# Kernel optimization log

Hardware: AMD Instinct MI355X
Metric: run time of the kernel (lower is better)

The kernel has to match this reference:

```python
import jax, jax.numpy as jnp
import numpy as np

N_NODES = 50000
N_EDGES = 800000
HEADS = 4
HID = 48
NEG_SLOPE = 0.2


def setup_inputs() -> dict:
    key = jax.random.key(0)
    ks = list(jax.random.split(key, 32))
    inp = {}
    inp['x'] = jax.random.normal(ks[0], (N_NODES, 3), dtype=jnp.float32)
    inp['edge_index'] = jax.random.randint(ks[1], (2, N_EDGES), 0, N_NODES, dtype=jnp.int64)
    dims = [3, HID, HID]
    ki = 2
    for li, din in enumerate(dims):
        s = 1.0 / np.sqrt(din)
        inp[f'Wl{li}'] = jax.random.normal(ks[ki], (din, HEADS * HID), dtype=jnp.float32) * s; ki += 1
        inp[f'bl{li}'] = jnp.zeros((HEADS * HID,), dtype=jnp.float32)
        inp[f'Wr{li}'] = jax.random.normal(ks[ki], (din, HEADS * HID), dtype=jnp.float32) * s; ki += 1
        inp[f'br{li}'] = jnp.zeros((HEADS * HID,), dtype=jnp.float32)
        inp[f'att{li}'] = jax.random.normal(ks[ki], (HEADS, HID), dtype=jnp.float32) * (1.0 / np.sqrt(HID)); ki += 1
        inp[f'bias{li}'] = jnp.zeros((HID,), dtype=jnp.float32)
    inp['head_w'] = jax.random.normal(ks[ki], (HID, 1), dtype=jnp.float32) * (1.0 / np.sqrt(HID))
    inp['head_b'] = jnp.full((1,), 0.1, dtype=jnp.float32)
    return inp


def _gatv2_layer(x, src, dst, Wl, bl, Wr, br, att, bias):
    # GATv2Conv, concat=False, eval mode (dropout off), self-loops already in (src,dst)
    N = x.shape[0]
    xl = (x @ Wl + bl).reshape(N, HEADS, HID)  # source transform
    xr = (x @ Wr + br).reshape(N, HEADS, HID)  # target transform
    e = jax.nn.leaky_relu(xl[src] + xr[dst], NEG_SLOPE)  # [E,H,C]
    score = jnp.einsum('ehc,hc->eh', e, att)             # [E,H]
    # segment softmax over edges grouped by destination node
    m = jax.ops.segment_max(score, dst, num_segments=N)
    p = jnp.exp(score - m[dst])
    denom = jax.ops.segment_sum(p, dst, num_segments=N)
    alpha = p / (denom[dst] + 1e-16)                     # [E,H]
    out = jax.ops.segment_sum(alpha[..., None] * xl[src], dst, num_segments=N)  # [N,H,C]
    return out.mean(axis=1) + bias  # concat=False -> mean over heads


def reference(x, edge_index, Wl0, bl0, Wr0, br0, att0, bias0,
              Wl1, bl1, Wr1, br1, att1, bias1,
              Wl2, bl2, Wr2, br2, att2, bias2, head_w, head_b):
    N = x.shape[0]
    loops = jnp.arange(N, dtype=edge_index.dtype)
    src = jnp.concatenate([edge_index[0], loops])  # PyG add_self_loops=True
    dst = jnp.concatenate([edge_index[1], loops])
    params = [(Wl0, bl0, Wr0, br0, att0, bias0),
              (Wl1, bl1, Wr1, br1, att1, bias1),
              (Wl2, bl2, Wr2, br2, att2, bias2)]
    for (Wl, bl, Wr, br, att, bias) in params:
        x = _gatv2_layer(x, src, dst, Wl, bl, Wr, br, att, bias)
        x = jax.nn.elu(x)
    out = (x @ head_w + head_b)[:, 0]
    return jax.nn.relu(out)
```

## Files before the change

### kernel.cpp

```cpp
#include <hip/hip_runtime.h>
#include <hip/hip_bf16.h>
#include <math.h>

#define HEADS 4
#define HID 48
#define FDIM 192
#define NEG_SLOPE 0.2f

typedef float f4 __attribute__((ext_vector_type(4)));

template<int CTRL>
__device__ __forceinline__ float dpp_add(float v) {
    int t = __builtin_amdgcn_update_dpp(0, __float_as_int(v), CTRL, 0xF, 0xF, true);
    return v + __int_as_float(t);
}
template<int CTRL>
__device__ __forceinline__ float dpp_max(float v) {
    int t = __builtin_amdgcn_update_dpp(0, __float_as_int(v), CTRL, 0xF, 0xF, true);
    return fmaxf(v, __int_as_float(t));
}
__device__ __forceinline__ float red_cq(float v) {
    v = dpp_add<0xB1>(v);
    v = dpp_add<0x4E>(v);
    return v;
}
__device__ __forceinline__ float red_es(float v) {
    v = dpp_add<0x124>(v);
    v = dpp_add<0x128>(v);
    return v;
}
__device__ __forceinline__ float rowmax16(float v) {
    v = dpp_max<0x124>(v);
    v = dpp_max<0x128>(v);
    return v;
}

__device__ __forceinline__ int detect64(const int* __restrict__ ei) {
    int l = (int)(threadIdx.x & 63);
    int v = ei[2 * l + 1];
    return (__ballot(v != 0) == 0ULL) ? 1 : 0;
}

__global__ void hist_kernel(const int* __restrict__ ei,
                            int* __restrict__ deg, int E, int E2) {
    int is64 = detect64(ei);
    for (int e = blockIdx.x * blockDim.x + threadIdx.x; e < E2;
         e += gridDim.x * blockDim.x) {
        int d;
        if (e < E) d = is64 ? ei[2 * (E + e)] : ei[E + e];
        else       d = e - E;
        atomicAdd(&deg[d], 1);
    }
}

__global__ void scan_local_kernel(const int* __restrict__ deg, int* __restrict__ incl,
                                  int* __restrict__ bsum, int N) {
    __shared__ int sm[256];
    int i = blockIdx.x * 256 + threadIdx.x;
    int v = (i < N) ? deg[i] : 0;
    sm[threadIdx.x] = v;
    __syncthreads();
    #pragma unroll
    for (int off = 1; off < 256; off <<= 1) {
        int t = ((int)threadIdx.x >= off) ? sm[threadIdx.x - off] : 0;
        __syncthreads();
        sm[threadIdx.x] += t;
        __syncthreads();
    }
    if (i < N) incl[i] = sm[threadIdx.x];
    if (threadIdx.x == 255) bsum[blockIdx.x] = sm[255];
}

__global__ void scan_bsum_kernel(int* __restrict__ bsum, int nb) {
    __shared__ int sm[256];
    __shared__ int running;
    if (threadIdx.x == 0) running = 0;
    __syncthreads();
    for (int base = 0; base < nb; base += 256) {
        int i = base + (int)threadIdx.x;
        int v = (i < nb) ? bsum[i] : 0;
        sm[threadIdx.x] = v;
        __syncthreads();
        #pragma unroll
        for (int off = 1; off < 256; off <<= 1) {
            int t = ((int)threadIdx.x >= off) ? sm[threadIdx.x - off] : 0;
            __syncthreads();
            sm[threadIdx.x] += t;
            __syncthreads();
        }
        if (i < nb) bsum[i] = running + sm[threadIdx.x] - v;
        __syncthreads();
        if (threadIdx.x == 0) running += sm[255];
        __syncthreads();
    }
}

__global__ void scan_final_kernel(const int* __restrict__ incl, const int* __restrict__ bsum,
                                  int* __restrict__ rowptr, int* __restrict__ cursor, int N) {
    int i = blockIdx.x * 256 + threadIdx.x;
    if (i < N) { rowptr[i + 1] = incl[i] + bsum[blockIdx.x]; cursor[i] = 0; }
    if (i == 0) rowptr[0] = 0;
}

__global__ void scatter_kernel(const int* __restrict__ ei,
                               const int* __restrict__ rowptr, int* __restrict__ cursor,
                               int* __restrict__ srcs, int E, int E2) {
    int is64 = detect64(ei);
    for (int e = blockIdx.x * blockDim.x + threadIdx.x; e < E2;
         e += gridDim.x * blockDim.x) {
        int s, d;
        if (e < E) {
            if (is64) { s = ei[2 * e]; d = ei[2 * (E + e)]; }
            else      { s = ei[e];     d = ei[E + e]; }
        } else {
            s = d = e - E;
        }
        int pos = rowptr[d] + atomicAdd(&cursor[d], 1);
        srcs[pos] = s;
    }
}

template<int DIN>
__global__ __launch_bounds__(192) void gemm2t_kernel(
    const float* __restrict__ xin,
    const float* __restrict__ Wl, const float* __restrict__ bl,
    const float* __restrict__ Wr, const float* __restrict__ br,
    float* __restrict__ xl, float* __restrict__ xr, int N) {
    int t  = (int)threadIdx.x;
    int cg = t % 48;
    int ng = t / 48;
    int c0 = cg * 4;
    int n0 = blockIdx.x * 16 + ng * 4;
    if (n0 >= N) return;

    f4 bLv = *(const f4*)&bl[c0];
    f4 bRv = *(const f4*)&br[c0];
    f4 accL[4], accR[4];
    #pragma unroll
    for (int i = 0; i < 4; ++i) { accL[i] = bLv; accR[i] = bRv; }

    if (n0 + 3 < N) {
        if (DIN == 3) {
            float xv[4][3];
            #pragma unroll
            for (int i = 0; i < 4; ++i) {
                const float* xp = xin + (size_t)(n0 + i) * 3;
                xv[i][0] = xp[0]; xv[i][1] = xp[1]; xv[i][2] = xp[2];
            }
            #pragma unroll
            for (int k = 0; k < 3; ++k) {
                f4 wl4 = *(const f4*)&Wl[k * FDIM + c0];
                f4 wr4 = *(const f4*)&Wr[k * FDIM + c0];
                #pragma unroll
                for (int i = 0; i < 4; ++i) {
                    float xs = xv[i][k];
                    accL[i] += xs * wl4;
                    accR[i] += xs * wr4;
                }
            }
        } else {
            #pragma unroll
            for (int kk = 0; kk < DIN; kk += 8) {
                float xv[4][8];
                #pragma unroll
                for (int i = 0; i < 4; ++i) {
                    const float* xp = xin + (size_t)(n0 + i) * DIN + kk;
                    f4 xa = *(const f4*)xp;
                    f4 xb = *(const f4*)(xp + 4);
                    #pragma unroll
                    for (int q = 0; q < 4; ++q) { xv[i][q] = xa[q]; xv[i][4 + q] = xb[q]; }
                }
                #pragma unroll
                for (int k = 0; k < 8; ++k) {
                    f4 wl4 = *(const f4*)&Wl[(kk + k) * FDIM + c0];
                    f4 wr4 = *(const f4*)&Wr[(kk + k) * FDIM + c0];
                    #pragma unroll
                    for (int i = 0; i < 4; ++i) {
                        float xs = xv[i][k];
                        accL[i] += xs * wl4;
                        accR[i] += xs * wr4;
                    }
                }
            }
        }
        #pragma unroll
        for (int i = 0; i < 4; ++i) {
            *(f4*)&xl[(size_t)(n0 + i) * FDIM + c0] = accL[i];
            *(f4*)&xr[(size_t)(n0 + i) * FDIM + c0] = accR[i];
        }
    } else {
        for (int i = 0; i < 4; ++i) {
            int n = n0 + i;
            if (n >= N) break;
            f4 aL = bLv;
            f4 aR = bRv;
            for (int k = 0; k < DIN; ++k) {
                float xs = xin[(size_t)n * DIN + k];
                f4 wl4 = *(const f4*)&Wl[k * FDIM + c0];
                f4 wr4 = *(const f4*)&Wr[k * FDIM + c0];
                aL += xs * wl4;
                aR += xs * wr4;
            }
            *(f4*)&xl[(size_t)n * FDIM + c0] = aL;
            *(f4*)&xr[(size_t)n * FDIM + c0] = aR;
        }
    }
}

#define SCORE_MASKED (-1e38f)
#define M_INIT       (-3e38f)
#define DEFER_THR    8.0f

__global__ __launch_bounds__(256) void gat_layer_kernel(
    const float* __restrict__ xl, const float* __restrict__ xr,
    const float* __restrict__ att, const float* __restrict__ bias,
    const int* __restrict__ rowptr, const int* __restrict__ srcs,
    float* __restrict__ xout,
    float* __restrict__ out,
    const float* __restrict__ head_w, const float* __restrict__ head_b,
    int N, int final_flag) {
    int wave = (int)((blockIdx.x * blockDim.x + threadIdx.x) >> 6);
    wave = __builtin_amdgcn_readfirstlane(wave);
    if (wave >= N) return;
    int lane = (int)(threadIdx.x & 63);
    int n  = wave;
    int h  = lane >> 4;
    int es = (lane >> 2) & 3;
    int cq = lane & 3;
    int j0 = h * HID + cq * 12;

    const float* xrp = xr + (size_t)n * FDIM + j0;
    f4 r0 = *(const f4*)xrp;
    f4 r1 = *(const f4*)(xrp + 4);
    f4 r2 = *(const f4*)(xrp + 8);
    f4 a0 = *(const f4*)&att[j0];
    f4 a1 = *(const f4*)&att[j0 + 4];
    f4 a2 = *(const f4*)&att[j0 + 8];

    float m = M_INIT, dn = 0.f;
    f4 acc0 = {0.f, 0.f, 0.f, 0.f}, acc1 = acc0, acc2 = acc0;

    int e0 = rowptr[n], e1 = rowptr[n + 1];
    int elast = e1 - 1;

    for (int e = e0; e < e1; e += 8) {
        int iA = e + es;
        int iB = e + 4 + es;
        int kA = (iA < e1) ? iA : elast;
        int kB = (iB < e1) ? iB : elast;
        int sA = srcs[kA];
        int sB = srcs[kB];
        const float* pA = xl + (size_t)sA * FDIM + j0;
        const float* pB = xl + (size_t)sB * FDIM + j0;
        f4 A0 = *(const f4*)pA, A1 = *(const f4*)(pA + 4), A2 = *(const f4*)(pA + 8);
        f4 B0 = *(const f4*)pB, B1 = *(const f4*)(pB + 4), B2 = *(const f4*)(pB + 8);

        float scA = 0.f, scB = 0.f;
        #pragma unroll
        for (int q = 0; q < 4; ++q) {
            float t, u;
            t = A0[q] + r0[q]; u = fmaf(NEG_SLOPE, fminf(t, 0.f), fmaxf(t, 0.f)); scA = fmaf(u, a0[q], scA);
            t = A1[q] + r1[q]; u = fmaf(NEG_SLOPE, fminf(t, 0.f), fmaxf(t, 0.f)); scA = fmaf(u, a1[q], scA);
            t = A2[q] + r2[q]; u = fmaf(NEG_SLOPE, fminf(t, 0.f), fmaxf(t, 0.f)); scA = fmaf(u, a2[q], scA);
            t = B0[q] + r0[q]; u = fmaf(NEG_SLOPE, fminf(t, 0.f), fmaxf(t, 0.f)); scB = fmaf(u, a0[q], scB);
            t = B1[q] + r1[q]; u = fmaf(NEG_SLOPE, fminf(t, 0.f), fmaxf(t, 0.f)); scB = fmaf(u, a1[q], scB);
            t = B2[q] + r2[q]; u = fmaf(NEG_SLOPE, fminf(t, 0.f), fmaxf(t, 0.f)); scB = fmaf(u, a2[q], scB);
        }
        scA = red_cq(scA);
        scB = red_cq(scB);
        scA = (iA < e1) ? scA : SCORE_MASKED;
        scB = (iB < e1) ? scB : SCORE_MASKED;

        float bmax = rowmax16(fmaxf(scA, scB));
        if (__any(bmax > m + DEFER_THR)) {
            float nm = fmaxf(m, bmax);
            float sc_ = __expf(m - nm);
            dn *= sc_; acc0 *= sc_; acc1 *= sc_; acc2 *= sc_;
            m = nm;
        }
        float qA = __expf(scA - m);
        float qB = __expf(scB - m);
        dn += qA + qB;
        acc0 += qA * A0 + qB * B0;
        acc1 += qA * A1 + qB * B1;
        acc2 += qA * A2 + qB * B2;
    }

    dn = red_es(dn);
    #pragma unroll
    for (int q = 0; q < 4; ++q) {
        acc0[q] = red_es(acc0[q]);
        acc1[q] = red_es(acc1[q]);
        acc2[q] = red_es(acc2[q]);
    }

    float inv = 1.0f / (dn + 1e-16f);
    f4 o0 = acc0 * inv, o1 = acc1 * inv, o2 = acc2 * inv;

    #pragma unroll
    for (int q = 0; q < 4; ++q) {
        float v;
        v = o0[q]; v += __shfl_xor(v, 16); v += __shfl_xor(v, 32); o0[q] = v;
        v = o1[q]; v += __shfl_xor(v, 16); v += __shfl_xor(v, 32); o1[q] = v;
        v = o2[q]; v += __shfl_xor(v, 16); v += __shfl_xor(v, 32); o2[q] = v;
    }
    int c0 = cq * 12;
    f4 b0v = *(const f4*)&bias[c0];
    f4 b1v = *(const f4*)&bias[c0 + 4];
    f4 b2v = *(const f4*)&bias[c0 + 8];
    o0 = 0.25f * o0 + b0v;
    o1 = 0.25f * o1 + b1v;
    o2 = 0.25f * o2 + b2v;
    #pragma unroll
    for (int q = 0; q < 4; ++q) {
        o0[q] = (o0[q] > 0.f) ? o0[q] : (__expf(o0[q]) - 1.f);
        o1[q] = (o1[q] > 0.f) ? o1[q] : (__expf(o1[q]) - 1.f);
        o2[q] = (o2[q] > 0.f) ? o2[q] : (__expf(o2[q]) - 1.f);
    }

    if (!final_flag) {
        if (h == 0 && es == 0) {
            float* xo = xout + (size_t)n * HID + c0;
            *(f4*)xo = o0;
            *(f4*)(xo + 4) = o1;
            *(f4*)(xo + 8) = o2;
        }
    } else {
        f4 w0 = *(const f4*)&head_w[c0];
        f4 w1 = *(const f4*)&head_w[c0 + 4];
        f4 w2 = *(const f4*)&head_w[c0 + 8];
        float part = 0.f;
        #pragma unroll
        for (int q = 0; q < 4; ++q)
            part += o0[q] * w0[q] + o1[q] * w1[q] + o2[q] * w2[q];
        part = red_cq(part);
        if (lane == 0) {
            float v = part + head_b[0];
            out[n] = (v > 0.f) ? v : 0.f;
        }
    }
}

extern "C" void kernel_launch(void* const* d_in, const int* in_sizes, int n_in,
                              void* d_out, int out_size, void* d_ws, size_t ws_size,
                              hipStream_t stream) {
    const float* x0 = (const float*)d_in[0];
    const int*   ei = (const int*)d_in[1];

    const int N  = in_sizes[0] / 3;
    const int E  = in_sizes[1] / 2;
    const int E2 = E + N;

    const float* Wl[3];  const float* bl[3];
    const float* Wr[3];  const float* br[3];
    const float* att[3]; const float* bias[3];
    for (int li = 0; li < 3; ++li) {
        int b = 2 + 6 * li;
        Wl[li]   = (const float*)d_in[b + 0];
        bl[li]   = (const float*)d_in[b + 1];
        Wr[li]   = (const float*)d_in[b + 2];
        br[li]   = (const float*)d_in[b + 3];
        att[li]  = (const float*)d_in[b + 4];
        bias[li] = (const float*)d_in[b + 5];
    }
    const float* head_w = (const float*)d_in[20];
    const float* head_b = (const float*)d_in[21];
    float* out = (float*)d_out;

    size_t off = 0;
    auto alloc = [&](size_t bytes) -> void* {
        void* p = (char*)d_ws + off;
        off = (off + bytes + 255) & ~(size_t)255;
        return p;
    };
    const int nb = (N + 255) / 256;
    int*   deg    = (int*)alloc((size_t)N * sizeof(int));
    int*   incl   = (int*)alloc((size_t)N * sizeof(int));
    int*   bsum   = (int*)alloc((size_t)nb * sizeof(int));
    int*   rowptr = (int*)alloc((size_t)(N + 1) * sizeof(int));
    int*   srcs   = (int*)alloc((size_t)E2 * sizeof(int));
    float* xlb    = (float*)alloc((size_t)N * FDIM * sizeof(float));
    float* xrb    = (float*)alloc((size_t)N * FDIM * sizeof(float));
    float* xbuf   = (float*)alloc((size_t)N * HID * sizeof(float));
    (void)ws_size;

    (void)hipMemsetAsync(deg, 0, (size_t)N * sizeof(int), stream);
    hist_kernel<<<2048, 256, 0, stream>>>(ei, deg, E, E2);
    scan_local_kernel<<<nb, 256, 0, stream>>>(deg, incl, bsum, N);
    scan_bsum_kernel<<<1, 256, 0, stream>>>(bsum, nb);
    scan_final_kernel<<<nb, 256, 0, stream>>>(incl, bsum, rowptr, deg, N);
    scatter_kernel<<<2048, 256, 0, stream>>>(ei, rowptr, deg, srcs, E, E2);

    const int waves_per_block = 4;
    int gat_blocks = (N + waves_per_block - 1) / waves_per_block;
    int gemm_blocks = (N + 15) / 16;

    gemm2t_kernel<3><<<gemm_blocks, 192, 0, stream>>>(x0, Wl[0], bl[0], Wr[0], br[0], xlb, xrb, N);
    gat_layer_kernel<<<gat_blocks, 256, 0, stream>>>(xlb, xrb, att[0], bias[0],
        rowptr, srcs, xbuf, nullptr, nullptr, nullptr, N, 0);

    gemm2t_kernel<HID><<<gemm_blocks, 192, 0, stream>>>(xbuf, Wl[1], bl[1], Wr[1], br[1], xlb, xrb, N);
    gat_layer_kernel<<<gat_blocks, 256, 0, stream>>>(xlb, xrb, att[1], bias[1],
        rowptr, srcs, xbuf, nullptr, nullptr, nullptr, N, 0);

    gemm2t_kernel<HID><<<gemm_blocks, 192, 0, stream>>>(xbuf, Wl[2], bl[2], Wr[2], br[2], xlb, xrb, N);
    gat_layer_kernel<<<gat_blocks, 256, 0, stream>>>(xlb, xrb, att[2], bias[2],
        rowptr, srcs, nullptr, out, head_w, head_b, N, 1);

    (void)n_in; (void)out_size;
}
```

Baseline: 490.2 us.

## Split GAT aggregation per head with head-major layout and XCD-aware block mapping

The projected features are stored head-major ([H][N][48]) instead of node-major, and the aggregation is split so each block handles a single head. Block IDs are mapped so that each pair of XCDs works on one head, which keeps each XCD's gather working set (one head's slice of xl) small enough to fit in its L2. Per-head partial results are combined with atomicAdd into a zeroed buffer. Separate combine kernels then apply bias and ELU, plus the output head in the last layer. The cost is extra launches and memsets, float atomics with non-deterministic summation order, and one edge per lane-group per iteration instead of two.

Result: slower. 1.571 ms (+220.5%).

```diff
diff --git a/kernel.cpp b/kernel.cpp
--- a/kernel.cpp
+++ b/kernel.cpp
@@ -24,14 +24,14 @@
     v = dpp_add<0x4E>(v);
     return v;
 }
-__device__ __forceinline__ float red_es(float v) {
-    v = dpp_add<0x124>(v);
-    v = dpp_add<0x128>(v);
-    return v;
-}
 __device__ __forceinline__ float rowmax16(float v) {
     v = dpp_max<0x124>(v);
     v = dpp_max<0x128>(v);
+    return v;
+}
+__device__ __forceinline__ float rowadd16(float v) {
+    v = dpp_add<0x124>(v);
+    v = dpp_add<0x128>(v);
     return v;
 }
 
@@ -132,6 +132,8 @@
     int c0 = cg * 4;
     int n0 = blockIdx.x * 16 + ng * 4;
     if (n0 >= N) return;
+    int hh = c0 / 48;
+    int ch = c0 - hh * 48;
 
     f4 bLv = *(const f4*)&bl[c0];
     f4 bRv = *(const f4*)&br[c0];
@@ -185,8 +187,9 @@
         }
         #pragma unroll
         for (int i = 0; i < 4; ++i) {
-            *(f4*)&xl[(size_t)(n0 + i) * FDIM + c0] = accL[i];
-            *(f4*)&xr[(size_t)(n0 + i) * FDIM + c0] = accR[i];
+            size_t o = ((size_t)hh * N + (n0 + i)) * HID + ch;
+            *(f4*)&xl[o] = accL[i];
+            *(f4*)&xr[o] = accR[i];
         }
     } else {
         for (int i = 0; i < 4; ++i) {
@@ -201,8 +204,9 @@
                 aL += xs * wl4;
                 aR += xs * wr4;
             }
-            *(f4*)&xl[(size_t)n * FDIM + c0] = aL;
-            *(f4*)&xr[(size_t)n * FDIM + c0] = aR;
+            size_t o = ((size_t)hh * N + n) * HID + ch;
+            *(f4*)&xl[o] = aL;
+            *(f4*)&xr[o] = aR;
         }
     }
 }
@@ -211,133 +215,149 @@
 #define M_INIT       (-3e38f)
 #define DEFER_THR    8.0f
 
-__global__ __launch_bounds__(256) void gat_layer_kernel(
-    const float* __restrict__ xl, const float* __restrict__ xr,
-    const float* __restrict__ att, const float* __restrict__ bias,
+__global__ __launch_bounds__(256) void gat_head_kernel(
+    const float* __restrict__ xlh,
+    const float* __restrict__ xrh,
+    const float* __restrict__ att,
     const int* __restrict__ rowptr, const int* __restrict__ srcs,
-    float* __restrict__ xout,
-    float* __restrict__ out,
-    const float* __restrict__ head_w, const float* __restrict__ head_b,
-    int N, int final_flag) {
-    int wave = (int)((blockIdx.x * blockDim.x + threadIdx.x) >> 6);
-    wave = __builtin_amdgcn_readfirstlane(wave);
-    if (wave >= N) return;
+    float* __restrict__ psum,
+    int N) {
+    int bid = (int)blockIdx.x;
+    int xcd = bid & 7;
+    int h   = xcd >> 1;
+    int j   = (bid >> 3) * 2 + (xcd & 1);
+    int wv  = (int)(threadIdx.x >> 6);
     int lane = (int)(threadIdx.x & 63);
-    int n  = wave;
-    int h  = lane >> 4;
-    int es = (lane >> 2) & 3;
-    int cq = lane & 3;
-    int j0 = h * HID + cq * 12;
-
-    const float* xrp = xr + (size_t)n * FDIM + j0;
+    int half = lane >> 5;
+    int l5 = lane & 31;
+    int es = l5 >> 2;
+    int cq = l5 & 3;
+    int c0 = cq * 12;
+    int n = j * 8 + wv * 2 + half;
+    bool nvalid = (n < N);
+    int nc = nvalid ? n : 0;
+
+    const float* hb = xlh + (size_t)h * N * HID;
+    const float* xrp = xrh + (size_t)h * N * HID + (size_t)nc * HID + c0;
     f4 r0 = *(const f4*)xrp;
     f4 r1 = *(const f4*)(xrp + 4);
     f4 r2 = *(const f4*)(xrp + 8);
-    f4 a0 = *(const f4*)&att[j0];
-    f4 a1 = *(const f4*)&att[j0 + 4];
-    f4 a2 = *(const f4*)&att[j0 + 8];
+    f4 a0 = *(const f4*)&att[h * HID + c0];
+    f4 a1 = *(const f4*)&att[h * HID + c0 + 4];
+    f4 a2 = *(const f4*)&att[h * HID + c0 + 8];
+
+    int e0 = nvalid ? rowptr[n] : 0;
+    int e1 = nvalid ? rowptr[n + 1] : 0;
+    int elast = e1 - 1;
 
     float m = M_INIT, dn = 0.f;
     f4 acc0 = {0.f, 0.f, 0.f, 0.f}, acc1 = acc0, acc2 = acc0;
 
-    int e0 = rowptr[n], e1 = rowptr[n + 1];
-    int elast = e1 - 1;
-
     for (int e = e0; e < e1; e += 8) {
-        int iA = e + es;
-        int iB = e + 4 + es;
-        int kA = (iA < e1) ? iA : elast;
-        int kB = (iB < e1) ? iB : elast;
-        int sA = srcs[kA];
-        int sB = srcs[kB];
-        const float* pA = xl + (size_t)sA * FDIM + j0;
-        const float* pB = xl + (size_t)sB * FDIM + j0;
-        f4 A0 = *(const f4*)pA, A1 = *(const f4*)(pA + 4), A2 = *(const f4*)(pA + 8);
-        f4 B0 = *(const f4*)pB, B1 = *(const f4*)(pB + 4), B2 = *(const f4*)(pB + 8);
-
-        float scA = 0.f, scB = 0.f;
+        int idx = e + es;
+        int k = (idx < e1) ? idx : elast;
+        int s = srcs[k];
+        const float* p = hb + (size_t)s * HID + c0;
+        f4 A0 = *(const f4*)p;
+        f4 A1 = *(const f4*)(p + 4);
+        f4 A2 = *(const f4*)(p + 8);
+
+        float sc = 0.f;
         #pragma unroll
         for (int q = 0; q < 4; ++q) {
-            float t, u;
-            t = A0[q] + r0[q]; u = fmaf(NEG_SLOPE, fminf(t, 0.f), fmaxf(t, 0.f)); scA = fmaf(u, a0[q], scA);
-            t = A1[q] + r1[q]; u = fmaf(NEG_SLOPE, fminf(t, 0.f), fmaxf(t, 0.f)); scA = fmaf(u, a1[q], scA);
-            t = A2[q] + r2[q]; u = fmaf(NEG_SLOPE, fminf(t, 0.f), fmaxf(t, 0.f)); scA = fmaf(u, a2[q], scA);
-            t = B0[q] + r0[q]; u = fmaf(NEG_SLOPE, fminf(t, 0.f), fmaxf(t, 0.f)); scB = fmaf(u, a0[q], scB);
-            t = B1[q] + r1[q]; u = fmaf(NEG_SLOPE, fminf(t, 0.f), fmaxf(t, 0.f)); scB = fmaf(u, a1[q], scB);
-            t = B2[q] + r2[q]; u = fmaf(NEG_SLOPE, fminf(t, 0.f), fmaxf(t, 0.f)); scB = fmaf(u, a2[q], scB);
-        }
-        scA = red_cq(scA);
-        scB = red_cq(scB);
-        scA = (iA < e1) ? scA : SCORE_MASKED;
-        scB = (iB < e1) ? scB : SCORE_MASKED;
-
-        float bmax = rowmax16(fmaxf(scA, scB));
+            float t;
+            t = A0[q] + r0[q]; sc = fmaf(fmaxf(t, NEG_SLOPE * t), a0[q], sc);
+            t = A1[q] + r1[q]; sc = fmaf(fmaxf(t, NEG_SLOPE * t), a1[q], sc);
+            t = A2[q] + r2[q]; sc = fmaf(fmaxf(t, NEG_SLOPE * t), a2[q], sc);
+        }
+        sc = red_cq(sc);
+        sc = (idx < e1) ? sc : SCORE_MASKED;
+
+        float bmax = rowmax16(sc);
+        bmax = fmaxf(bmax, __shfl_xor(bmax, 16));
         if (__any(bmax > m + DEFER_THR)) {
             float nm = fmaxf(m, bmax);
-            float sc_ = __expf(m - nm);
-            dn *= sc_; acc0 *= sc_; acc1 *= sc_; acc2 *= sc_;
+            float s_ = __expf(m - nm);
+            dn *= s_; acc0 *= s_; acc1 *= s_; acc2 *= s_;
             m = nm;
         }
-        float qA = __expf(scA - m);
-        float qB = __expf(scB - m);
-        dn += qA + qB;
-        acc0 += qA * A0 + qB * B0;
-        acc1 += qA * A1 + qB * B1;
-        acc2 += qA * A2 + qB * B2;
-    }
-
-    dn = red_es(dn);
-    #pragma unroll
-    for (int q = 0; q < 4; ++q) {
-        acc0[q] = red_es(acc0[q]);
-        acc1[q] = red_es(acc1[q]);
-        acc2[q] = red_es(acc2[q]);
-    }
-
-    float inv = 1.0f / (dn + 1e-16f);
-    f4 o0 = acc0 * inv, o1 = acc1 * inv, o2 = acc2 * inv;
-
+        float q_ = __expf(sc - m);
+        dn += q_;
+        acc0 += q_ * A0;
+        acc1 += q_ * A1;
+        acc2 += q_ * A2;
+    }
+
+    dn = rowadd16(dn); dn += __shfl_xor(dn, 16);
     #pragma unroll
     for (int q = 0; q < 4; ++q) {
         float v;
-        v = o0[q]; v += __shfl_xor(v, 16); v += __shfl_xor(v, 32); o0[q] = v;
-        v = o1[q]; v += __shfl_xor(v, 16); v += __shfl_xor(v, 32); o1[q] = v;
-        v = o2[q]; v += __shfl_xor(v, 16); v += __shfl_xor(v, 32); o2[q] = v;
-    }
+        v = rowadd16(acc0[q]); v += __shfl_xor(v, 16); acc0[q] = v;
+        v = rowadd16(acc1[q]); v += __shfl_xor(v, 16); acc1[q] = v;
+        v = rowadd16(acc2[q]); v += __shfl_xor(v, 16); acc2[q] = v;
+    }
+
+    if (nvalid && es == 0) {
+        float w = 0.25f / (dn + 1e-16f);
+        float* po = psum + (size_t)n * HID + c0;
+        #pragma unroll
+        for (int q = 0; q < 4; ++q) {
+            atomicAdd(&po[q],     acc0[q] * w);
+            atomicAdd(&po[4 + q], acc1[q] * w);
+            atomicAdd(&po[8 + q], acc2[q] * w);
+        }
+    }
+}
+
+__global__ void combine_kernel(float* __restrict__ psum,
+                               const float* __restrict__ bias, int N) {
+    int t = blockIdx.x * 256 + threadIdx.x;
+    int n = t >> 2, cq = t & 3;
+    if (n >= N) return;
     int c0 = cq * 12;
-    f4 b0v = *(const f4*)&bias[c0];
-    f4 b1v = *(const f4*)&bias[c0 + 4];
-    f4 b2v = *(const f4*)&bias[c0 + 8];
-    o0 = 0.25f * o0 + b0v;
-    o1 = 0.25f * o1 + b1v;
-    o2 = 0.25f * o2 + b2v;
+    float* p = psum + (size_t)n * HID + c0;
+    f4 v0 = *(const f4*)p + *(const f4*)&bias[c0];
+    f4 v1 = *(const f4*)(p + 4) + *(const f4*)&bias[c0 + 4];
+    f4 v2 = *(const f4*)(p + 8) + *(const f4*)&bias[c0 + 8];
     #pragma unroll
     for (int q = 0; q < 4; ++q) {
-        o0[q] = (o0[q] > 0.f) ? o0[q] : (__expf(o0[q]) - 1.f);
-        o1[q] = (o1[q] > 0.f) ? o1[q] : (__expf(o1[q]) - 1.f);
-        o2[q] = (o2[q] > 0.f) ? o2[q] : (__expf(o2[q]) - 1.f);
-    }
-
-    if (!final_flag) {
-        if (h == 0 && es == 0) {
-            float* xo = xout + (size_t)n * HID + c0;
-            *(f4*)xo = o0;
-            *(f4*)(xo + 4) = o1;
-            *(f4*)(xo + 8) = o2;
-        }
-    } else {
-        f4 w0 = *(const f4*)&head_w[c0];
-        f4 w1 = *(const f4*)&head_w[c0 + 4];
-        f4 w2 = *(const f4*)&head_w[c0 + 8];
-        float part = 0.f;
-        #pragma unroll
-        for (int q = 0; q < 4; ++q)
-            part += o0[q] * w0[q] + o1[q] * w1[q] + o2[q] * w2[q];
-        part = red_cq(part);
-        if (lane == 0) {
-            float v = part + head_b[0];
-            out[n] = (v > 0.f) ? v : 0.f;
-        }
+        v0[q] = (v0[q] > 0.f) ? v0[q] : (__expf(v0[q]) - 1.f);
+        v1[q] = (v1[q] > 0.f) ? v1[q] : (__expf(v1[q]) - 1.f);
+        v2[q] = (v2[q] > 0.f) ? v2[q] : (__expf(v2[q]) - 1.f);
+    }
+    *(f4*)p = v0;
+    *(f4*)(p + 4) = v1;
+    *(f4*)(p + 8) = v2;
+}
+
+__global__ void combine_final_kernel(const float* __restrict__ psum,
+                                     const float* __restrict__ bias,
+                                     const float* __restrict__ head_w,
+                                     const float* __restrict__ head_b,
+                                     float* __restrict__ out, int N) {
+    int t = blockIdx.x * 256 + threadIdx.x;
+    int n = t >> 2, cq = t & 3;
+    if (n >= N) return;
+    int c0 = cq * 12;
+    const float* p = psum + (size_t)n * HID + c0;
+    f4 v0 = *(const f4*)p + *(const f4*)&bias[c0];
+    f4 v1 = *(const f4*)(p + 4) + *(const f4*)&bias[c0 + 4];
+    f4 v2 = *(const f4*)(p + 8) + *(const f4*)&bias[c0 + 8];
+    f4 w0 = *(const f4*)&head_w[c0];
+    f4 w1 = *(const f4*)&head_w[c0 + 4];
+    f4 w2 = *(const f4*)&head_w[c0 + 8];
+    float d = 0.f;
+    #pragma unroll
+    for (int q = 0; q < 4; ++q) {
+        float e0 = (v0[q] > 0.f) ? v0[q] : (__expf(v0[q]) - 1.f);
+        float e1 = (v1[q] > 0.f) ? v1[q] : (__expf(v1[q]) - 1.f);
+        float e2 = (v2[q] > 0.f) ? v2[q] : (__expf(v2[q]) - 1.f);
+        d += e0 * w0[q] + e1 * w1[q] + e2 * w2[q];
+    }
+    d = red_cq(d);
+    if (cq == 0) {
+        float v = d + head_b[0];
+        out[n] = (v > 0.f) ? v : 0.f;
     }
 }
 
@@ -381,7 +401,7 @@
     int*   srcs   = (int*)alloc((size_t)E2 * sizeof(int));
     float* xlb    = (float*)alloc((size_t)N * FDIM * sizeof(float));
     float* xrb    = (float*)alloc((size_t)N * FDIM * sizeof(float));
-    float* xbuf   = (float*)alloc((size_t)N * HID * sizeof(float));
+    float* psum   = (float*)alloc((size_t)N * HID * sizeof(float));
     (void)ws_size;
 
     (void)hipMemsetAsync(deg, 0, (size_t)N * sizeof(int), stream);
@@ -391,21 +411,25 @@
     scan_final_kernel<<<nb, 256, 0, stream>>>(incl, bsum, rowptr, deg, N);
     scatter_kernel<<<2048, 256, 0, stream>>>(ei, rowptr, deg, srcs, E, E2);
 
-    const int waves_per_block = 4;
-    int gat_blocks = (N + waves_per_block - 1) / waves_per_block;
     int gemm_blocks = (N + 15) / 16;
-
+    int gat_blocks  = ((((N + 7) / 8) + 1) / 2) * 8;
+    int cmb_blocks  = (N * 4 + 255) / 256;
+    size_t psum_bytes = (size_t)N * HID * sizeof(float);
+
+    (void)hipMemsetAsync(psum, 0, psum_bytes, stream);
     gemm2t_kernel<3><<<gemm_blocks, 192, 0, stream>>>(x0, Wl[0], bl[0], Wr[0], br[0], xlb, xrb, N);
-    gat_layer_kernel<<<gat_blocks, 256, 0, stream>>>(xlb, xrb, att[0], bias[0],
-        rowptr, srcs, xbuf, nullptr, nullptr, nullptr, N, 0);
-
-    gemm2t_kernel<HID><<<gemm_blocks, 192, 0, stream>>>(xbuf, Wl[1], bl[1], Wr[1], br[1], xlb, xrb, N);
-    gat_layer_kernel<<<gat_blocks, 256, 0, stream>>>(xlb, xrb, att[1], bias[1],
-        rowptr, srcs, xbuf, nullptr, nullptr, nullptr, N, 0);
-
-    gemm2t_kernel<HID><<<gemm_blocks, 192, 0, stream>>>(xbuf, Wl[2], bl[2], Wr[2], br[2], xlb, xrb, N);
-    gat_layer_kernel<<<gat_blocks, 256, 0, stream>>>(xlb, xrb, att[2], bias[2],
-        rowptr, srcs, nullptr, out, head_w, head_b, N, 1);
+    gat_head_kernel<<<gat_blocks, 256, 0, stream>>>(xlb, xrb, att[0], rowptr, srcs, psum, N);
+    combine_kernel<<<cmb_blocks, 256, 0, stream>>>(psum, bias[0], N);
+
+    gemm2t_kernel<HID><<<gemm_blocks, 192, 0, stream>>>(psum, Wl[1], bl[1], Wr[1], br[1], xlb, xrb, N);
+    (void)hipMemsetAsync(psum, 0, psum_bytes, stream);
+    gat_head_kernel<<<gat_blocks, 256, 0, stream>>>(xlb, xrb, att[1], rowptr, srcs, psum, N);
+    combine_kernel<<<cmb_blocks, 256, 0, stream>>>(psum, bias[1], N);
+
+    gemm2t_kernel<HID><<<gemm_blocks, 192, 0, stream>>>(psum, Wl[2], bl[2], Wr[2], br[2], xlb, xrb, N);
+    (void)hipMemsetAsync(psum, 0, psum_bytes, stream);
+    gat_head_kernel<<<gat_blocks, 256, 0, stream>>>(xlb, xrb, att[2], rowptr, srcs, psum, N);
+    combine_final_kernel<<<cmb_blocks, 256, 0, stream>>>(psum, bias[2], head_w, head_b, out, N);
 
     (void)n_in; (void)out_size;
 }
```
